# Optimization experiments

Measured on AMD Instinct MI355X. Metric: run time of the kernel, lower is better.

Reference implementation:

```python
import jax, jax.numpy as jnp
import numpy as np

R = 8192        # proposals per image
D = 4096        # box-head feature dim (input_shape.channels)
C = 80          # num_classes (COCO)
K_PRE = 512     # per-class pre-NMS top-k candidates
IMG_W, IMG_H = 1000.0, 800.0
SCORE_THRESH = 1e-5
NMS_THRESH = 0.5
TOPK = 100      # test_topk_per_image


def setup_inputs() -> dict:
    key = jax.random.key(0)
    ks = jax.random.split(key, 6)
    x = jax.random.normal(ks[0], (R, D), jnp.float32)
    # Xavier-uniform init for the two linear heads
    lim = np.sqrt(6.0 / (D + C)).astype(np.float32)
    Wc = jax.random.uniform(ks[1], (D, C), jnp.float32, -lim, lim)
    bc = jnp.zeros((C,), jnp.float32)
    Wd = jax.random.uniform(ks[2], (D, C), jnp.float32, -lim, lim)
    bd = jnp.zeros((C,), jnp.float32)
    # class-agnostic proposal boxes in xyxy, roughly inside the image
    xy = jax.random.uniform(ks[3], (R, 2), jnp.float32) * jnp.array([IMG_W * 0.8, IMG_H * 0.8], jnp.float32)
    wh = jax.random.uniform(ks[4], (R, 2), jnp.float32) * jnp.array([IMG_W * 0.3, IMG_H * 0.3], jnp.float32) + 4.0
    boxes = jnp.concatenate([xy, xy + wh], axis=1)
    return {"x": x, "Wc": Wc, "bc": bc, "Wd": Wd, "bd": bd, "boxes": boxes}


def _pairwise_iou(b):  # b: [K,4] xyxy -> [K,K]
    area = (b[:, 2] - b[:, 0]) * (b[:, 3] - b[:, 1])
    lt = jnp.maximum(b[:, None, :2], b[None, :, :2])
    rb = jnp.minimum(b[:, None, 2:], b[None, :, 2:])
    wh = jnp.clip(rb - lt, 0.0)
    inter = wh[..., 0] * wh[..., 1]
    return inter / (area[:, None] + area[None, :] - inter + 1e-9)


def _nms_one_class(scores_c, boxes):  # scores_c: [R], boxes: [R,4] -> keep mask [R]
    vals, idx = jax.lax.top_k(scores_c, K_PRE)          # pre-NMS top-k, score-sorted desc
    iou = _pairwise_iou(boxes[idx])                      # [K_PRE, K_PRE]
    valid = vals > SCORE_THRESH                          # score thresholding

    def body(kept, i):
        # suppressed if any already-kept higher-scoring box overlaps too much
        sup = jnp.any(kept & (iou[i] > NMS_THRESH))
        k = valid[i] & (~sup)
        return kept.at[i].set(k), k

    _, keeps = jax.lax.scan(body, jnp.zeros((K_PRE,), bool), jnp.arange(K_PRE))
    return jnp.zeros((scores_c.shape[0],), bool).at[idx].set(keeps)


def _clip_boxes(boxes):
    x1 = jnp.clip(boxes[:, 0:1], 0.0, IMG_W)
    y1 = jnp.clip(boxes[:, 1:2], 0.0, IMG_H)
    x2 = jnp.clip(boxes[:, 2:3], 0.0, IMG_W)
    y2 = jnp.clip(boxes[:, 3:4], 0.0, IMG_H)
    return jnp.concatenate([x1, y1, x2, y2], axis=1)


def reference(x, Wc, bc, Wd, bd, boxes):
    # WSDDN-style object-mining head: softmax over classes x softmax over proposals
    cls_logits = x @ Wc + bc                    # [R, C]
    det_logits = x @ Wd + bd                    # [R, C]
    pred = jax.nn.softmax(cls_logits, axis=1) * jax.nn.softmax(det_logits, axis=0)

    # inference path: clip boxes, threshold, per-class (batched) NMS, keep topk
    bclip = _clip_boxes(boxes)
    keep = jax.vmap(_nms_one_class, in_axes=(1, None), out_axes=1)(pred, bclip)  # [R, C]
    kept_scores = jnp.where(keep, pred, 0.0)
    # topk_per_image across all (proposal, class) detections
    kth = jax.lax.top_k(kept_scores.reshape(-1), TOPK)[0][-1]
    return jnp.where(kept_scores >= kth, kept_scores, 0.0)   # [R, C]
```

## Files before the change

kernel.cpp:

```cpp
#include <hip/hip_runtime.h>
#include <hip/hip_bf16.h>
#include <math.h>

#define R_N 8192
#define D_K 4096
#define C_N 80
#define NC2 160
#define KSPLIT 8
#define KSLICE (D_K / KSPLIT)
#define KPRE 512
#define TOPK 100
#define LIST_CAP (80 * 512)

typedef _Float16 f16;
typedef f16 f16x8 __attribute__((ext_vector_type(8)));
typedef float f32x4 __attribute__((ext_vector_type(4)));

__device__ __forceinline__ void async_copy16(const void* g, void* l) {
    __builtin_amdgcn_global_load_lds(
        (const __attribute__((address_space(1))) void*)g,
        (__attribute__((address_space(3))) void*)l, 16, 0, 0);
}

__global__ __launch_bounds__(256) void zero_kernel(float* __restrict__ out, unsigned* __restrict__ cnt) {
    int idx = blockIdx.x * 256 + threadIdx.x;
    if (idx < R_N * C_N) out[idx] = 0.0f;
    if (blockIdx.x == 0 && threadIdx.x == 0) *cnt = 0u;
}

__global__ __launch_bounds__(256) void wt_convert(const float* __restrict__ Wc,
                                                  const float* __restrict__ Wd,
                                                  f16* __restrict__ BhT,
                                                  f16* __restrict__ BlT) {
    const int n = blockIdx.x;
    const float* src = (n < C_N) ? (Wc + n) : (Wd + (n - C_N));
    f16* dh = BhT + (size_t)n * D_K;
    f16* dl = BlT + (size_t)n * D_K;
    for (int k = threadIdx.x; k < D_K; k += 256) {
        float v = src[(size_t)k * C_N];
        f16 h = (f16)v;
        dh[k] = h;
        dl[k] = (f16)(v - (float)h);
    }
}

__global__ __launch_bounds__(256) void gemm_part(const float* __restrict__ x,
                                                 const f16* __restrict__ BhT,
                                                 const f16* __restrict__ BlT,
                                                 float* __restrict__ part) {
    __shared__ __align__(16) float As[128 * 32];
    __shared__ __align__(16) f16 Bhs[160 * 32];
    __shared__ __align__(16) f16 Bls[160 * 32];

    const int b    = blockIdx.x;
    const int rb   = b & 63;
    const int ks   = b >> 6;
    const int row0 = rb * 128;
    const int kbase = ks * KSLICE;
    const int tid  = threadIdx.x;
    const int wv   = tid >> 6, lane = tid & 63;
    const int m    = lane & 15, quad = lane >> 4;

    f32x4 acc[2][10];
#pragma unroll
    for (int t = 0; t < 2; ++t)
#pragma unroll
        for (int n = 0; n < 10; ++n) acc[t][n] = (f32x4)(0.0f);

    for (int ch = 0; ch < KSLICE / 32; ++ch) {
        const int k0 = kbase + ch * 32;
#pragma unroll
        for (int i = 0; i < 4; ++i) {
            int t = tid + 256 * i;
            int r = t >> 3, cs = t & 7;
            int cg = cs ^ (r & 7);
            async_copy16(x + (size_t)(row0 + r) * D_K + k0 + cg * 4,
                         (char*)As + (size_t)t * 16);
        }
#pragma unroll
        for (int i = 0; i < 3; ++i) {
            int t = tid + 256 * i;
            if (t < 640) {
                int nn = t >> 2, cc = t & 3;
                size_t go = (size_t)nn * D_K + k0 + cc * 8;
                async_copy16(BhT + go, (char*)Bhs + (size_t)t * 16);
                async_copy16(BlT + go, (char*)Bls + (size_t)t * 16);
            }
        }
        __syncthreads();
        f16x8 ah[2], al[2];
#pragma unroll
        for (int t = 0; t < 2; ++t) {
            int r = wv * 32 + t * 16 + m;
            int r7 = r & 7;
            float4 c0 = *(const float4*)&As[r * 32 + (((2 * quad) ^ r7) << 2)];
            float4 c1 = *(const float4*)&As[r * 32 + (((2 * quad + 1) ^ r7) << 2)];
            float tv[8] = {c0.x, c0.y, c0.z, c0.w, c1.x, c1.y, c1.z, c1.w};
#pragma unroll
            for (int j = 0; j < 8; ++j) {
                f16 h = (f16)tv[j];
                ah[t][j] = h;
                al[t][j] = (f16)(tv[j] - (float)h);
            }
        }
#pragma unroll
        for (int n = 0; n < 10; ++n) {
            int nn = n * 16 + m;
            f16x8 bh = *(const f16x8*)&Bhs[nn * 32 + quad * 8];
            f16x8 bl = *(const f16x8*)&Bls[nn * 32 + quad * 8];
#pragma unroll
            for (int t = 0; t < 2; ++t) {
                acc[t][n] = __builtin_amdgcn_mfma_f32_16x16x32_f16(al[t], bh, acc[t][n], 0, 0, 0);
                acc[t][n] = __builtin_amdgcn_mfma_f32_16x16x32_f16(ah[t], bl, acc[t][n], 0, 0, 0);
                acc[t][n] = __builtin_amdgcn_mfma_f32_16x16x32_f16(ah[t], bh, acc[t][n], 0, 0, 0);
            }
        }
        __syncthreads();
    }
#pragma unroll
    for (int t = 0; t < 2; ++t) {
        int grow0 = row0 + wv * 32 + t * 16 + quad * 4;
#pragma unroll
        for (int n = 0; n < 10; ++n) {
            int gcol = n * 16 + m;
#pragma unroll
            for (int r4 = 0; r4 < 4; ++r4)
                part[((size_t)ks * R_N + grow0 + r4) * NC2 + gcol] = acc[t][n][r4];
        }
    }
}

__global__ __launch_bounds__(256) void reduce_bias(const float* __restrict__ part,
                                                   const float* __restrict__ bc,
                                                   const float* __restrict__ bd,
                                                   float* __restrict__ cls,
                                                   float* __restrict__ detT) {
    const size_t STRIDE = (size_t)R_N * NC2;
    size_t idx = (size_t)blockIdx.x * 256 + threadIdx.x;
    int row = (int)(idx / NC2), col = (int)(idx % NC2);
    float p0 = part[idx + 0 * STRIDE], p1 = part[idx + 1 * STRIDE];
    float p2 = part[idx + 2 * STRIDE], p3 = part[idx + 3 * STRIDE];
    float p4 = part[idx + 4 * STRIDE], p5 = part[idx + 5 * STRIDE];
    float p6 = part[idx + 6 * STRIDE], p7 = part[idx + 7 * STRIDE];
    float s = ((p0 + p1) + (p2 + p3)) + ((p4 + p5) + (p6 + p7));
    if (col < C_N) {
        cls[(size_t)row * C_N + col] = s + bc[col];
    } else {
        detT[(size_t)(col - C_N) * R_N + row] = s + bd[col - C_N];
    }
}

__global__ __launch_bounds__(256) void row_softmax(const float* __restrict__ cls,
                                                   float* __restrict__ P) {
    int tid = threadIdx.x;
    int wave = tid >> 6, lane = tid & 63;
    int row = blockIdx.x * 4 + wave;
    float v0 = cls[(size_t)row * C_N + lane];
    float v1 = (lane < 16) ? cls[(size_t)row * C_N + 64 + lane] : -INFINITY;
    float m = fmaxf(v0, v1);
#pragma unroll
    for (int off = 32; off > 0; off >>= 1) m = fmaxf(m, __shfl_xor(m, off, 64));
    float e0 = expf(v0 - m);
    float e1 = (lane < 16) ? expf(v1 - m) : 0.0f;
    float s = e0 + e1;
#pragma unroll
    for (int off = 32; off > 0; off >>= 1) s += __shfl_xor(s, off, 64);
    P[(size_t)lane * R_N + row] = e0 / s;
    if (lane < 16) P[(size_t)(64 + lane) * R_N + row] = e1 / s;
}

__global__ __launch_bounds__(256) void col_softmax_mul(const float* __restrict__ detT,
                                                       float* __restrict__ P) {
    __shared__ float red[256];
    int c = blockIdx.x, tid = threadIdx.x;
    const float* dc = detT + (size_t)c * R_N;
    float m = -INFINITY;
    for (int r = tid; r < R_N; r += 256) m = fmaxf(m, dc[r]);
    red[tid] = m; __syncthreads();
    for (int s2 = 128; s2 > 0; s2 >>= 1) {
        if (tid < s2) red[tid] = fmaxf(red[tid], red[tid + s2]);
        __syncthreads();
    }
    m = red[0]; __syncthreads();
    float sum = 0.0f;
    for (int r = tid; r < R_N; r += 256) sum += expf(dc[r] - m);
    red[tid] = sum; __syncthreads();
    for (int s2 = 128; s2 > 0; s2 >>= 1) {
        if (tid < s2) red[tid] += red[tid + s2];
        __syncthreads();
    }
    float s = red[0];
    float* pc = P + (size_t)c * R_N;
    for (int r = tid; r < R_N; r += 256) pc[r] = pc[r] * (expf(dc[r] - m) / s);
}

__global__ __launch_bounds__(256) void chunk_sort(const float* __restrict__ P,
                                                  unsigned long long* __restrict__ cand) {
    __shared__ unsigned long long sk[1024];
    const int c = blockIdx.x >> 3, ch = blockIdx.x & 7;
    const int tid = threadIdx.x;
    const float* pc = P + (size_t)c * R_N + ch * 1024;

    for (int i = tid; i < 1024; i += 256) {
        unsigned u = __float_as_uint(pc[i]);
        int r = ch * 1024 + i;
        sk[i] = ((unsigned long long)u << 32) | (unsigned)(8191 - r);
    }
    __syncthreads();
    for (int size = 2; size <= 1024; size <<= 1) {
        for (int stride = size >> 1; stride > 0; stride >>= 1) {
            for (int t = tid; t < 512; t += 256) {
                int i = 2 * t - (t & (stride - 1));
                int j = i + stride;
                unsigned long long a = sk[i], b = sk[j];
                bool desc = ((i & size) == 0);
                if ((a < b) == desc) { sk[i] = b; sk[j] = a; }
            }
            __syncthreads();
        }
    }
    unsigned long long* dst = cand + (size_t)blockIdx.x * 512;
    for (int i = tid; i < 512; i += 256) dst[i] = sk[i];
}

__global__ __launch_bounds__(256) void merge_extract(const unsigned long long* __restrict__ cand,
                                                     const float* __restrict__ boxes,
                                                     float* __restrict__ svals,
                                                     int* __restrict__ sridx,
                                                     float* __restrict__ cbox,
                                                     int* __restrict__ nvalid) {
    __shared__ unsigned long long A[1024];
    const int c = blockIdx.x, tid = threadIdx.x;
    const unsigned long long* base = cand + (size_t)c * 8 * 512;

    for (int i = tid; i < 512; i += 256) A[i] = base[i];
    for (int l = 1; l < 8; ++l) {
        __syncthreads();
        for (int i = tid; i < 512; i += 256) A[512 + i] = base[l * 512 + (511 - i)];
        __syncthreads();
        for (int stride = 512; stride > 0; stride >>= 1) {
            for (int t = tid; t < 512; t += 256) {
                int i = 2 * t - (t & (stride - 1));
                int j = i + stride;
                unsigned long long a = A[i], b = A[j];
                if (a < b) { A[i] = b; A[j] = a; }
            }
            __syncthreads();
        }
    }
    __syncthreads();
    for (int i = tid; i < 512; i += 256) {
        unsigned long long k = A[i];
        float v = __uint_as_float((unsigned)(k >> 32));
        int r = 8191 - (int)(k & 0xFFFFFFFFull);
        svals[c * 512 + i] = v;
        sridx[c * 512 + i] = r;
        float b0 = boxes[r * 4 + 0], b1 = boxes[r * 4 + 1];
        float b2 = boxes[r * 4 + 2], b3 = boxes[r * 4 + 3];
        float4 cb;
        cb.x = fminf(fmaxf(b0, 0.0f), 1000.0f);
        cb.y = fminf(fmaxf(b1, 0.0f), 800.0f);
        cb.z = fminf(fmaxf(b2, 0.0f), 1000.0f);
        cb.w = fminf(fmaxf(b3, 0.0f), 800.0f);
        *(float4*)&cbox[((size_t)c * 512 + i) * 4] = cb;
        float vn = (i < 511) ? __uint_as_float((unsigned)(A[i + 1] >> 32)) : -1.0f;
        if (v > 1e-5f && !(vn > 1e-5f)) nvalid[c] = i + 1;
        if (i == 0 && !(v > 1e-5f)) nvalid[c] = 0;
    }
}

__global__ __launch_bounds__(256) void iou_mask(const float* __restrict__ cbox,
                                                const int* __restrict__ nvalid,
                                                unsigned long long* __restrict__ gmask) {
    __shared__ float sx1[512], sy1[512], sx2[512], sy2[512], sar[512];
    const int c = blockIdx.x >> 3, w = blockIdx.x & 7;
    const int tid = threadIdx.x;
    const int nv = nvalid[c];

    for (int i = tid; i < 512; i += 256) {
        float4 b = *(const float4*)&cbox[((size_t)c * 512 + i) * 4];
        sx1[i] = b.x; sy1[i] = b.y; sx2[i] = b.z; sy2[i] = b.w;
        sar[i] = (b.z - b.x) * (b.w - b.y);
    }
    __syncthreads();
    for (int i = tid; i < 512; i += 256) {
        unsigned long long bits = 0ull;
        if (i < nv && w <= (i >> 6)) {
            float xi1 = sx1[i], yi1 = sy1[i], xi2 = sx2[i], yi2 = sy2[i], ai = sar[i];
#pragma unroll 8
            for (int j2 = 0; j2 < 64; ++j2) {
                int j = (w << 6) + j2;
                float xx1 = fmaxf(xi1, sx1[j]);
                float yy1 = fmaxf(yi1, sy1[j]);
                float xx2 = fminf(xi2, sx2[j]);
                float yy2 = fminf(yi2, sy2[j]);
                float ww = fmaxf(xx2 - xx1, 0.0f);
                float hh = fmaxf(yy2 - yy1, 0.0f);
                float inter = ww * hh;
                float iou = inter / (ai + sar[j] - inter + 1e-9f);
                if (iou > 0.5f) bits |= (1ull << j2);
            }
        }
        gmask[((size_t)c * 512 + i) * 8 + w] = bits;
    }
}

__global__ __launch_bounds__(64) void nms_scan(const unsigned long long* __restrict__ gmask,
                                               const float* __restrict__ svals,
                                               const int* __restrict__ sridx,
                                               const int* __restrict__ nvalid,
                                               float* __restrict__ g_ls,
                                               unsigned* __restrict__ g_lp,
                                               unsigned* __restrict__ g_cnt,
                                               float* __restrict__ k100) {
    __shared__ unsigned long long sm[512 * 8];
    __shared__ unsigned char keepf[512];
    const int c = blockIdx.x, lane = threadIdx.x;
    const int nv = nvalid[c];
    const unsigned long long* gm = gmask + (size_t)c * 512 * 8;

    for (int t = lane; t < 4096; t += 64) sm[t] = gm[t];
    __syncthreads();

    const bool rd = (lane < 8);
    unsigned long long keptw = 0ull;
    unsigned long long pf[8];
#pragma unroll
    for (int d = 0; d < 8; ++d) pf[d] = rd ? sm[(d & 511) * 8 + lane] : 0ull;
    for (int i = 0; i < nv; ++i) {
        unsigned long long mm = pf[i & 7];
        int ip = (i + 8) & 511;
        pf[i & 7] = rd ? sm[ip * 8 + lane] : 0ull;
        int sup = __any((keptw & mm) != 0ull);
        int keep = !sup;
        if (keep && lane == (i >> 6)) keptw |= (1ull << (i & 63));
        if (lane == 0) keepf[i] = (unsigned char)keep;
    }
    __syncthreads();
    for (int i = lane; i < nv; i += 64) {
        if (keepf[i]) {
            unsigned pos = atomicAdd(g_cnt, 1u);
            g_ls[pos] = svals[c * 512 + i];
            g_lp[pos] = (unsigned)(sridx[c * 512 + i] * C_N + c);
        }
    }
    for (int i = lane; i < 100; i += 64) k100[c * 100 + i] = 0.0f;
    unsigned base = 0;
    for (int ch2 = 0; ch2 < 8 && (int)base < 100; ++ch2) {
        int i = ch2 * 64 + lane;
        bool kk = (i < nv) && (keepf[i] != 0);
        unsigned long long mb = __ballot(kk);
        unsigned pre = (unsigned)__popcll(mb & ((1ull << lane) - 1ull));
        if (kk && base + pre < 100)
            k100[c * 100 + base + pre] = svals[c * 512 + i];
        base += (unsigned)__popcll(mb);
    }
}

__global__ __launch_bounds__(256) void kth_kernel(const float* __restrict__ k100,
                                                  float* __restrict__ g_kth) {
    __shared__ unsigned red[4];
    __shared__ unsigned s_total;
    const int tid = threadIdx.x;
    const int wv = tid >> 6, lane = tid & 63;
    unsigned v[32];
#pragma unroll
    for (int j = 0; j < 32; ++j) {
        int idx = j * 256 + tid;
        v[j] = (idx < C_N * 100) ? __float_as_uint(k100[idx]) : 0u;
    }
    unsigned lo = 0u, hi = 0x7FFFFFFFu;
    while (lo < hi) {
        unsigned mid = lo + (hi - lo + 1) / 2;
        unsigned cnt = 0;
#pragma unroll
        for (int j = 0; j < 32; ++j) cnt += (v[j] >= mid) ? 1u : 0u;
#pragma unroll
        for (int off = 32; off > 0; off >>= 1) cnt += __shfl_down(cnt, off, 64);
        if (lane == 0) red[wv] = cnt;
        __syncthreads();
        if (tid == 0) s_total = red[0] + red[1] + red[2] + red[3];
        __syncthreads();
        unsigned total = s_total;
        if (total >= (unsigned)TOPK) lo = mid; else hi = mid - 1;
    }
    if (tid == 0) *g_kth = __uint_as_float(lo);
}

__global__ __launch_bounds__(256) void scatter_kernel(const float* __restrict__ g_ls,
                                                      const unsigned* __restrict__ g_lp,
                                                      const unsigned* __restrict__ g_cnt,
                                                      const float* __restrict__ g_kth,
                                                      float* __restrict__ out) {
    unsigned idx = blockIdx.x * 256 + threadIdx.x;
    unsigned n = *g_cnt;
    float kth = *g_kth;
    if (idx < n) {
        float s = g_ls[idx];
        if (s >= kth) out[g_lp[idx]] = s;
    }
}

extern "C" void kernel_launch(void* const* d_in, const int* in_sizes, int n_in,
                              void* d_out, int out_size, void* d_ws, size_t ws_size,
                              hipStream_t stream) {
    const float* x     = (const float*)d_in[0];
    const float* Wc    = (const float*)d_in[1];
    const float* bc    = (const float*)d_in[2];
    const float* Wd    = (const float*)d_in[3];
    const float* bd    = (const float*)d_in[4];
    const float* boxes = (const float*)d_in[5];
    float* out = (float*)d_out;

    char* w = (char*)d_ws;
    float* part = (float*)w;  w += (size_t)KSPLIT * R_N * NC2 * sizeof(float);
    float* cls  = (float*)w;  w += (size_t)R_N * C_N * sizeof(float);
    float* detT = (float*)w;  w += (size_t)C_N * R_N * sizeof(float);
    float* P    = (float*)w;  w += (size_t)C_N * R_N * sizeof(float);
    float* g_ls = (float*)w;  w += (size_t)LIST_CAP * sizeof(float);
    unsigned* g_lp = (unsigned*)w; w += (size_t)LIST_CAP * sizeof(unsigned);
    unsigned* g_cnt = (unsigned*)w; w += 256;
    float* g_kth = (float*)w; w += 256;
    f16* BhT = (f16*)w; w += (size_t)NC2 * D_K * sizeof(f16);
    f16* BlT = (f16*)w; w += (size_t)NC2 * D_K * sizeof(f16);
    float* k100 = (float*)w; w += (size_t)C_N * 100 * sizeof(float);

    char* a = (char*)part;
    unsigned long long* cand = (unsigned long long*)a; a += (size_t)C_N * 8 * 512 * sizeof(unsigned long long);
    float* svals = (float*)a;  a += (size_t)C_N * KPRE * sizeof(float);
    int*   sridx = (int*)a;    a += (size_t)C_N * KPRE * sizeof(int);
    float* cbox  = (float*)a;  a += (size_t)C_N * KPRE * 4 * sizeof(float);
    int*   nvalid = (int*)a;   a += 4096;
    unsigned long long* gmask = (unsigned long long*)a; a += (size_t)C_N * KPRE * 8 * sizeof(unsigned long long);

    zero_kernel<<<(R_N * C_N) / 256, 256, 0, stream>>>(out, g_cnt);
    wt_convert<<<NC2, 256, 0, stream>>>(Wc, Wd, BhT, BlT);
    gemm_part<<<64 * KSPLIT, 256, 0, stream>>>(x, BhT, BlT, part);
    reduce_bias<<<(R_N * NC2) / 256, 256, 0, stream>>>(part, bc, bd, cls, detT);
    row_softmax<<<R_N / 4, 256, 0, stream>>>(cls, P);
    col_softmax_mul<<<C_N, 256, 0, stream>>>(detT, P);
    chunk_sort<<<C_N * 8, 256, 0, stream>>>(P, cand);
    merge_extract<<<C_N, 256, 0, stream>>>(cand, boxes, svals, sridx, cbox, nvalid);
    iou_mask<<<C_N * 8, 256, 0, stream>>>(cbox, nvalid, gmask);
    nms_scan<<<C_N, 64, 0, stream>>>(gmask, svals, sridx, nvalid, g_ls, g_lp, g_cnt, k100);
    kth_kernel<<<1, 256, 0, stream>>>(k100, g_kth);
    scatter_kernel<<<(LIST_CAP + 255) / 256, 256, 0, stream>>>(g_ls, g_lp, g_cnt, g_kth, out);
}
```

Baseline: 391.9 us.

## Fuse init, softmax-multiply, and merge/IoU/NMS kernels; retile GEMM waves 2x2

Merges the output zeroing and the weight conversion into one init kernel, and rewrites the weight transpose to use coalesced float4 loads staged through shared memory. The GEMM wave layout changes from 1x4 rows to 2x2 (64 rows by 80 cols per wave), so each wave loads fewer B fragments from shared memory. The column softmax now only computes statistics, and the multiply is folded into chunk_sort, which removes one full pass over P. Merge, IoU mask and the NMS scan are fused into a single per-class kernel that keeps the masks in shared memory, cutting launches and global round-trips, but only 80 blocks do the IoU work.

```diff
diff --git a/kernel.cpp b/kernel.cpp
--- a/kernel.cpp
+++ b/kernel.cpp
@@ -13,8 +13,10 @@
 #define LIST_CAP (80 * 512)
 
 typedef _Float16 f16;
+typedef f16 f16x2 __attribute__((ext_vector_type(2)));
 typedef f16 f16x8 __attribute__((ext_vector_type(8)));
 typedef float f32x4 __attribute__((ext_vector_type(4)));
+typedef unsigned long long u64;
 
 __device__ __forceinline__ void async_copy16(const void* g, void* l) {
     __builtin_amdgcn_global_load_lds(
@@ -22,25 +24,41 @@
         (__attribute__((address_space(3))) void*)l, 16, 0, 0);
 }
 
-__global__ __launch_bounds__(256) void zero_kernel(float* __restrict__ out, unsigned* __restrict__ cnt) {
-    int idx = blockIdx.x * 256 + threadIdx.x;
-    if (idx < R_N * C_N) out[idx] = 0.0f;
-    if (blockIdx.x == 0 && threadIdx.x == 0) *cnt = 0u;
-}
-
-__global__ __launch_bounds__(256) void wt_convert(const float* __restrict__ Wc,
-                                                  const float* __restrict__ Wd,
-                                                  f16* __restrict__ BhT,
-                                                  f16* __restrict__ BlT) {
-    const int n = blockIdx.x;
-    const float* src = (n < C_N) ? (Wc + n) : (Wd + (n - C_N));
-    f16* dh = BhT + (size_t)n * D_K;
-    f16* dl = BlT + (size_t)n * D_K;
-    for (int k = threadIdx.x; k < D_K; k += 256) {
-        float v = src[(size_t)k * C_N];
-        f16 h = (f16)v;
-        dh[k] = h;
-        dl[k] = (f16)(v - (float)h);
+__global__ __launch_bounds__(256) void init_kernel(const float* __restrict__ Wc,
+                                                   const float* __restrict__ Wd,
+                                                   float* __restrict__ out,
+                                                   unsigned* __restrict__ cnt,
+                                                   f16* __restrict__ BhT,
+                                                   f16* __restrict__ BlT) {
+    const int b = blockIdx.x, tid = threadIdx.x;
+    if (b < 640) {
+        ((float4*)out)[b * 256 + tid] = make_float4(0.f, 0.f, 0.f, 0.f);
+        if (b == 0 && tid == 0) *cnt = 0u;
+        return;
+    }
+    __shared__ float Ws[32 * 161];
+    const int kb = b - 640;
+    const int k0 = kb * 32;
+    for (int i = tid; i < 1280; i += 256) {
+        int row = i / 40, q = i % 40;
+        const float* src = (q < 20) ? (Wc + (size_t)(k0 + row) * C_N + q * 4)
+                                    : (Wd + (size_t)(k0 + row) * C_N + (q - 20) * 4);
+        float4 t4 = *(const float4*)src;
+        int cc = (q < 20) ? q * 4 : 80 + (q - 20) * 4;
+        Ws[row * 161 + cc + 0] = t4.x; Ws[row * 161 + cc + 1] = t4.y;
+        Ws[row * 161 + cc + 2] = t4.z; Ws[row * 161 + cc + 3] = t4.w;
+    }
+    __syncthreads();
+    const int g = tid >> 4, l = tid & 15;
+#pragma unroll
+    for (int p = 0; p < 10; ++p) {
+        int n = p * 16 + g;
+        float v0 = Ws[(2 * l) * 161 + n];
+        float v1 = Ws[(2 * l + 1) * 161 + n];
+        f16 h0 = (f16)v0, h1 = (f16)v1;
+        f16 l0 = (f16)(v0 - (float)h0), l1 = (f16)(v1 - (float)h1);
+        *(f16x2*)&BhT[(size_t)n * D_K + k0 + 2 * l] = (f16x2){h0, h1};
+        *(f16x2*)&BlT[(size_t)n * D_K + k0 + 2 * l] = (f16x2){l0, l1};
     }
 }
 
@@ -59,13 +77,14 @@
     const int kbase = ks * KSLICE;
     const int tid  = threadIdx.x;
     const int wv   = tid >> 6, lane = tid & 63;
+    const int wm   = wv & 1, wn = wv >> 1;
     const int m    = lane & 15, quad = lane >> 4;
 
-    f32x4 acc[2][10];
-#pragma unroll
-    for (int t = 0; t < 2; ++t)
-#pragma unroll
-        for (int n = 0; n < 10; ++n) acc[t][n] = (f32x4)(0.0f);
+    f32x4 acc[4][5];
+#pragma unroll
+    for (int t = 0; t < 4; ++t)
+#pragma unroll
+        for (int n = 0; n < 5; ++n) acc[t][n] = (f32x4)(0.0f);
 
     for (int ch = 0; ch < KSLICE / 32; ++ch) {
         const int k0 = kbase + ch * 32;
@@ -88,10 +107,10 @@
             }
         }
         __syncthreads();
-        f16x8 ah[2], al[2];
-#pragma unroll
-        for (int t = 0; t < 2; ++t) {
-            int r = wv * 32 + t * 16 + m;
+        f16x8 ah[4], al[4];
+#pragma unroll
+        for (int t = 0; t < 4; ++t) {
+            int r = wm * 64 + t * 16 + m;
             int r7 = r & 7;
             float4 c0 = *(const float4*)&As[r * 32 + (((2 * quad) ^ r7) << 2)];
             float4 c1 = *(const float4*)&As[r * 32 + (((2 * quad + 1) ^ r7) << 2)];
@@ -104,12 +123,12 @@
             }
         }
 #pragma unroll
-        for (int n = 0; n < 10; ++n) {
-            int nn = n * 16 + m;
+        for (int n = 0; n < 5; ++n) {
+            int nn = (wn * 5 + n) * 16 + m;
             f16x8 bh = *(const f16x8*)&Bhs[nn * 32 + quad * 8];
             f16x8 bl = *(const f16x8*)&Bls[nn * 32 + quad * 8];
 #pragma unroll
-            for (int t = 0; t < 2; ++t) {
+            for (int t = 0; t < 4; ++t) {
                 acc[t][n] = __builtin_amdgcn_mfma_f32_16x16x32_f16(al[t], bh, acc[t][n], 0, 0, 0);
                 acc[t][n] = __builtin_amdgcn_mfma_f32_16x16x32_f16(ah[t], bl, acc[t][n], 0, 0, 0);
                 acc[t][n] = __builtin_amdgcn_mfma_f32_16x16x32_f16(ah[t], bh, acc[t][n], 0, 0, 0);
@@ -118,11 +137,11 @@
         __syncthreads();
     }
 #pragma unroll
-    for (int t = 0; t < 2; ++t) {
-        int grow0 = row0 + wv * 32 + t * 16 + quad * 4;
-#pragma unroll
-        for (int n = 0; n < 10; ++n) {
-            int gcol = n * 16 + m;
+    for (int t = 0; t < 4; ++t) {
+        int grow0 = row0 + wm * 64 + t * 16 + quad * 4;
+#pragma unroll
+        for (int n = 0; n < 5; ++n) {
+            int gcol = (wn * 5 + n) * 16 + m;
 #pragma unroll
             for (int r4 = 0; r4 < 4; ++r4)
                 part[((size_t)ks * R_N + grow0 + r4) * NC2 + gcol] = acc[t][n][r4];
@@ -151,7 +170,7 @@
 }
 
 __global__ __launch_bounds__(256) void row_softmax(const float* __restrict__ cls,
-                                                   float* __restrict__ P) {
+                                                   float* __restrict__ Pt) {
     int tid = threadIdx.x;
     int wave = tid >> 6, lane = tid & 63;
     int row = blockIdx.x * 4 + wave;
@@ -165,12 +184,13 @@
     float s = e0 + e1;
 #pragma unroll
     for (int off = 32; off > 0; off >>= 1) s += __shfl_xor(s, off, 64);
-    P[(size_t)lane * R_N + row] = e0 / s;
-    if (lane < 16) P[(size_t)(64 + lane) * R_N + row] = e1 / s;
-}
-
-__global__ __launch_bounds__(256) void col_softmax_mul(const float* __restrict__ detT,
-                                                       float* __restrict__ P) {
+    Pt[(size_t)lane * R_N + row] = e0 / s;
+    if (lane < 16) Pt[(size_t)(64 + lane) * R_N + row] = e1 / s;
+}
+
+__global__ __launch_bounds__(256) void col_stats(const float* __restrict__ detT,
+                                                 float* __restrict__ cm,
+                                                 float* __restrict__ csum) {
     __shared__ float red[256];
     int c = blockIdx.x, tid = threadIdx.x;
     const float* dc = detT + (size_t)c * R_N;
@@ -189,22 +209,26 @@
         if (tid < s2) red[tid] += red[tid + s2];
         __syncthreads();
     }
-    float s = red[0];
-    float* pc = P + (size_t)c * R_N;
-    for (int r = tid; r < R_N; r += 256) pc[r] = pc[r] * (expf(dc[r] - m) / s);
-}
-
-__global__ __launch_bounds__(256) void chunk_sort(const float* __restrict__ P,
+    if (tid == 0) { cm[c] = m; csum[c] = red[0]; }
+}
+
+__global__ __launch_bounds__(256) void chunk_sort(const float* __restrict__ Pt,
+                                                  const float* __restrict__ detT,
+                                                  const float* __restrict__ cm,
+                                                  const float* __restrict__ csum,
                                                   unsigned long long* __restrict__ cand) {
-    __shared__ unsigned long long sk[1024];
+    __shared__ u64 sk[1024];
     const int c = blockIdx.x >> 3, ch = blockIdx.x & 7;
     const int tid = threadIdx.x;
-    const float* pc = P + (size_t)c * R_N + ch * 1024;
+    const float m = cm[c], s = csum[c];
+    const float* pc = Pt + (size_t)c * R_N + ch * 1024;
+    const float* dc = detT + (size_t)c * R_N + ch * 1024;
 
     for (int i = tid; i < 1024; i += 256) {
-        unsigned u = __float_as_uint(pc[i]);
+        float val = pc[i] * (expf(dc[i] - m) / s);
+        unsigned u = __float_as_uint(val);
         int r = ch * 1024 + i;
-        sk[i] = ((unsigned long long)u << 32) | (unsigned)(8191 - r);
+        sk[i] = ((u64)u << 32) | (unsigned)(8191 - r);
     }
     __syncthreads();
     for (int size = 2; size <= 1024; size <<= 1) {
@@ -212,37 +236,43 @@
             for (int t = tid; t < 512; t += 256) {
                 int i = 2 * t - (t & (stride - 1));
                 int j = i + stride;
-                unsigned long long a = sk[i], b = sk[j];
+                u64 a = sk[i], b = sk[j];
                 bool desc = ((i & size) == 0);
                 if ((a < b) == desc) { sk[i] = b; sk[j] = a; }
             }
             __syncthreads();
         }
     }
-    unsigned long long* dst = cand + (size_t)blockIdx.x * 512;
+    u64* dst = cand + (size_t)blockIdx.x * 512;
     for (int i = tid; i < 512; i += 256) dst[i] = sk[i];
 }
 
-__global__ __launch_bounds__(256) void merge_extract(const unsigned long long* __restrict__ cand,
-                                                     const float* __restrict__ boxes,
-                                                     float* __restrict__ svals,
-                                                     int* __restrict__ sridx,
-                                                     float* __restrict__ cbox,
-                                                     int* __restrict__ nvalid) {
-    __shared__ unsigned long long A[1024];
+__global__ __launch_bounds__(256) void merge_nms(const u64* __restrict__ cand,
+                                                 const float* __restrict__ boxes,
+                                                 float* __restrict__ g_ls,
+                                                 unsigned* __restrict__ g_lp,
+                                                 unsigned* __restrict__ g_cnt,
+                                                 float* __restrict__ k100) {
+    __shared__ u64 A[1024];
+    __shared__ float sx1[512], sy1[512], sx2[512], sy2[512], sar[512], svals[512];
+    __shared__ int sridx[512];
+    __shared__ u64 msk[512 * 8];
+    __shared__ unsigned char keepf[512];
+    __shared__ int s_nv;
+
     const int c = blockIdx.x, tid = threadIdx.x;
-    const unsigned long long* base = cand + (size_t)c * 8 * 512;
+    const u64* base = cand + (size_t)c * 8 * 512;
 
     for (int i = tid; i < 512; i += 256) A[i] = base[i];
-    for (int l = 1; l < 8; ++l) {
-        __syncthreads();
-        for (int i = tid; i < 512; i += 256) A[512 + i] = base[l * 512 + (511 - i)];
+    for (int l2 = 1; l2 < 8; ++l2) {
+        __syncthreads();
+        for (int i = tid; i < 512; i += 256) A[512 + i] = base[l2 * 512 + (511 - i)];
         __syncthreads();
         for (int stride = 512; stride > 0; stride >>= 1) {
             for (int t = tid; t < 512; t += 256) {
                 int i = 2 * t - (t & (stride - 1));
                 int j = i + stride;
-                unsigned long long a = A[i], b = A[j];
+                u64 a = A[i], b = A[j];
                 if (a < b) { A[i] = b; A[j] = a; }
             }
             __syncthreads();
@@ -250,41 +280,27 @@
     }
     __syncthreads();
     for (int i = tid; i < 512; i += 256) {
-        unsigned long long k = A[i];
+        u64 k = A[i];
         float v = __uint_as_float((unsigned)(k >> 32));
         int r = 8191 - (int)(k & 0xFFFFFFFFull);
-        svals[c * 512 + i] = v;
-        sridx[c * 512 + i] = r;
+        svals[i] = v; sridx[i] = r;
         float b0 = boxes[r * 4 + 0], b1 = boxes[r * 4 + 1];
         float b2 = boxes[r * 4 + 2], b3 = boxes[r * 4 + 3];
-        float4 cb;
-        cb.x = fminf(fmaxf(b0, 0.0f), 1000.0f);
-        cb.y = fminf(fmaxf(b1, 0.0f), 800.0f);
-        cb.z = fminf(fmaxf(b2, 0.0f), 1000.0f);
-        cb.w = fminf(fmaxf(b3, 0.0f), 800.0f);
-        *(float4*)&cbox[((size_t)c * 512 + i) * 4] = cb;
+        float x1 = fminf(fmaxf(b0, 0.0f), 1000.0f);
+        float y1 = fminf(fmaxf(b1, 0.0f), 800.0f);
+        float x2 = fminf(fmaxf(b2, 0.0f), 1000.0f);
+        float y2 = fminf(fmaxf(b3, 0.0f), 800.0f);
+        sx1[i] = x1; sy1[i] = y1; sx2[i] = x2; sy2[i] = y2;
+        sar[i] = (x2 - x1) * (y2 - y1);
         float vn = (i < 511) ? __uint_as_float((unsigned)(A[i + 1] >> 32)) : -1.0f;
-        if (v > 1e-5f && !(vn > 1e-5f)) nvalid[c] = i + 1;
-        if (i == 0 && !(v > 1e-5f)) nvalid[c] = 0;
-    }
-}
-
-__global__ __launch_bounds__(256) void iou_mask(const float* __restrict__ cbox,
-                                                const int* __restrict__ nvalid,
-                                                unsigned long long* __restrict__ gmask) {
-    __shared__ float sx1[512], sy1[512], sx2[512], sy2[512], sar[512];
-    const int c = blockIdx.x >> 3, w = blockIdx.x & 7;
-    const int tid = threadIdx.x;
-    const int nv = nvalid[c];
-
-    for (int i = tid; i < 512; i += 256) {
-        float4 b = *(const float4*)&cbox[((size_t)c * 512 + i) * 4];
-        sx1[i] = b.x; sy1[i] = b.y; sx2[i] = b.z; sy2[i] = b.w;
-        sar[i] = (b.z - b.x) * (b.w - b.y);
-    }
-    __syncthreads();
-    for (int i = tid; i < 512; i += 256) {
-        unsigned long long bits = 0ull;
+        if (v > 1e-5f && !(vn > 1e-5f)) s_nv = i + 1;
+        if (i == 0 && !(v > 1e-5f)) s_nv = 0;
+    }
+    __syncthreads();
+    const int nv = s_nv;
+    for (int task = tid; task < 512 * 8; task += 256) {
+        int i = task >> 3, w = task & 7;
+        u64 bits = 0ull;
         if (i < nv && w <= (i >> 6)) {
             float xi1 = sx1[i], yi1 = sy1[i], xi2 = sx2[i], yi2 = sy2[i], ai = sar[i];
 #pragma unroll 8
@@ -301,59 +317,44 @@
                 if (iou > 0.5f) bits |= (1ull << j2);
             }
         }
-        gmask[((size_t)c * 512 + i) * 8 + w] = bits;
-    }
-}
-
-__global__ __launch_bounds__(64) void nms_scan(const unsigned long long* __restrict__ gmask,
-                                               const float* __restrict__ svals,
-                                               const int* __restrict__ sridx,
-                                               const int* __restrict__ nvalid,
-                                               float* __restrict__ g_ls,
-                                               unsigned* __restrict__ g_lp,
-                                               unsigned* __restrict__ g_cnt,
-                                               float* __restrict__ k100) {
-    __shared__ unsigned long long sm[512 * 8];
-    __shared__ unsigned char keepf[512];
-    const int c = blockIdx.x, lane = threadIdx.x;
-    const int nv = nvalid[c];
-    const unsigned long long* gm = gmask + (size_t)c * 512 * 8;
-
-    for (int t = lane; t < 4096; t += 64) sm[t] = gm[t];
-    __syncthreads();
-
-    const bool rd = (lane < 8);
-    unsigned long long keptw = 0ull;
-    unsigned long long pf[8];
-#pragma unroll
-    for (int d = 0; d < 8; ++d) pf[d] = rd ? sm[(d & 511) * 8 + lane] : 0ull;
-    for (int i = 0; i < nv; ++i) {
-        unsigned long long mm = pf[i & 7];
-        int ip = (i + 8) & 511;
-        pf[i & 7] = rd ? sm[ip * 8 + lane] : 0ull;
-        int sup = __any((keptw & mm) != 0ull);
-        int keep = !sup;
-        if (keep && lane == (i >> 6)) keptw |= (1ull << (i & 63));
-        if (lane == 0) keepf[i] = (unsigned char)keep;
-    }
-    __syncthreads();
-    for (int i = lane; i < nv; i += 64) {
+        msk[i * 8 + w] = bits;
+    }
+    __syncthreads();
+    if (tid < 64) {
+        const int lane = tid;
+        const bool rd = (lane < 8);
+        u64 keptw = 0ull;
+        u64 pf[8];
+#pragma unroll
+        for (int d = 0; d < 8; ++d) pf[d] = rd ? msk[(d & 511) * 8 + lane] : 0ull;
+        for (int i = 0; i < nv; ++i) {
+            u64 mm = pf[i & 7];
+            int ip = (i + 8) & 511;
+            pf[i & 7] = rd ? msk[ip * 8 + lane] : 0ull;
+            int sup = __any((keptw & mm) != 0ull);
+            int keep = !sup;
+            if (keep && lane == (i >> 6)) keptw |= (1ull << (i & 63));
+            if (lane == 0) keepf[i] = (unsigned char)keep;
+        }
+        for (int i = lane; i < 100; i += 64) k100[c * 100 + i] = 0.0f;
+        unsigned base2 = 0;
+        for (int ch2 = 0; ch2 < 8 && (int)base2 < 100; ++ch2) {
+            int i = ch2 * 64 + lane;
+            bool kk = (i < nv) && (keepf[i] != 0);
+            u64 mb = __ballot(kk);
+            unsigned pre = (unsigned)__popcll(mb & ((1ull << lane) - 1ull));
+            if (kk && base2 + pre < 100)
+                k100[c * 100 + base2 + pre] = svals[i];
+            base2 += (unsigned)__popcll(mb);
+        }
+    }
+    __syncthreads();
+    for (int i = tid; i < nv; i += 256) {
         if (keepf[i]) {
             unsigned pos = atomicAdd(g_cnt, 1u);
-            g_ls[pos] = svals[c * 512 + i];
-            g_lp[pos] = (unsigned)(sridx[c * 512 + i] * C_N + c);
-        }
-    }
-    for (int i = lane; i < 100; i += 64) k100[c * 100 + i] = 0.0f;
-    unsigned base = 0;
-    for (int ch2 = 0; ch2 < 8 && (int)base < 100; ++ch2) {
-        int i = ch2 * 64 + lane;
-        bool kk = (i < nv) && (keepf[i] != 0);
-        unsigned long long mb = __ballot(kk);
-        unsigned pre = (unsigned)__popcll(mb & ((1ull << lane) - 1ull));
-        if (kk && base + pre < 100)
-            k100[c * 100 + base + pre] = svals[c * 512 + i];
-        base += (unsigned)__popcll(mb);
+            g_ls[pos] = svals[i];
+            g_lp[pos] = (unsigned)(sridx[i] * C_N + c);
+        }
     }
 }
 
@@ -416,7 +417,7 @@
     float* part = (float*)w;  w += (size_t)KSPLIT * R_N * NC2 * sizeof(float);
     float* cls  = (float*)w;  w += (size_t)R_N * C_N * sizeof(float);
     float* detT = (float*)w;  w += (size_t)C_N * R_N * sizeof(float);
-    float* P    = (float*)w;  w += (size_t)C_N * R_N * sizeof(float);
+    float* Pt   = (float*)w;  w += (size_t)C_N * R_N * sizeof(float);
     float* g_ls = (float*)w;  w += (size_t)LIST_CAP * sizeof(float);
     unsigned* g_lp = (unsigned*)w; w += (size_t)LIST_CAP * sizeof(unsigned);
     unsigned* g_cnt = (unsigned*)w; w += 256;
@@ -424,25 +425,18 @@
     f16* BhT = (f16*)w; w += (size_t)NC2 * D_K * sizeof(f16);
     f16* BlT = (f16*)w; w += (size_t)NC2 * D_K * sizeof(f16);
     float* k100 = (float*)w; w += (size_t)C_N * 100 * sizeof(float);
-
-    char* a = (char*)part;
-    unsigned long long* cand = (unsigned long long*)a; a += (size_t)C_N * 8 * 512 * sizeof(unsigned long long);
-    float* svals = (float*)a;  a += (size_t)C_N * KPRE * sizeof(float);
-    int*   sridx = (int*)a;    a += (size_t)C_N * KPRE * sizeof(int);
-    float* cbox  = (float*)a;  a += (size_t)C_N * KPRE * 4 * sizeof(float);
-    int*   nvalid = (int*)a;   a += 4096;
-    unsigned long long* gmask = (unsigned long long*)a; a += (size_t)C_N * KPRE * 8 * sizeof(unsigned long long);
-
-    zero_kernel<<<(R_N * C_N) / 256, 256, 0, stream>>>(out, g_cnt);
-    wt_convert<<<NC2, 256, 0, stream>>>(Wc, Wd, BhT, BlT);
+    float* cm   = (float*)w; w += 1024;
+    float* csum = (float*)w; w += 1024;
+
+    u64* cand = (u64*)part;
+
+    init_kernel<<<768, 256, 0, stream>>>(Wc, Wd, out, g_cnt, BhT, BlT);
     gemm_part<<<64 * KSPLIT, 256, 0, stream>>>(x, BhT, BlT, part);
     reduce_bias<<<(R_N * NC2) / 256, 256, 0, stream>>>(part, bc, bd, cls, detT);
-    row_softmax<<<R_N / 4, 256, 0, stream>>>(cls, P);
-    col_softmax_mul<<<C_N, 256, 0, stream>>>(detT, P);
-    chunk_sort<<<C_N * 8, 256, 0, stream>>>(P, cand);
-    merge_extract<<<C_N, 256, 0, stream>>>(cand, boxes, svals, sridx, cbox, nvalid);
-    iou_mask<<<C_N * 8, 256, 0, stream>>>(cbox, nvalid, gmask);
-    nms_scan<<<C_N, 64, 0, stream>>>(gmask, svals, sridx, nvalid, g_ls, g_lp, g_cnt, k100);
+    row_softmax<<<R_N / 4, 256, 0, stream>>>(cls, Pt);
+    col_stats<<<C_N, 256, 0, stream>>>(detT, cm, csum);
+    chunk_sort<<<C_N * 8, 256, 0, stream>>>(Pt, detT, cm, csum, cand);
+    merge_nms<<<C_N, 256, 0, stream>>>(cand, boxes, g_ls, g_lp, g_cnt, k100);
     kth_kernel<<<1, 256, 0, stream>>>(k100, g_kth);
     scatter_kernel<<<(LIST_CAP + 255) / 256, 256, 0, stream>>>(g_ls, g_lp, g_cnt, g_kth, out);
 }
```

New measurement: 404.9 us. 3.3% more time.
